# Kernel optimization log

Hardware: AMD Instinct MI355X
Metric: run time of the kernel (lower is better)

The kernel has to match this reference:

```python
import jax, jax.numpy as jnp
import numpy as np

EPS = 1e-5

def _ln(v, g, b):
    m = v.mean(-1, keepdims=True)
    var = ((v - m) ** 2).mean(-1, keepdims=True)
    return (v - m) * jax.lax.rsqrt(var + EPS) * g + b

def _causal_dwconv(x, w, b):
    # x: [B,S,C], w: [C,K] depthwise kernel, b: [C]; causal (left) padding
    K = w.shape[1]
    xt = x.transpose(0, 2, 1)  # [B,C,S]
    out = jax.lax.conv_general_dilated(xt, w[:, None, :], (1,), [(K - 1, 0)],
                                       dimension_numbers=('NCH', 'OIH', 'NCH'),
                                       feature_group_count=w.shape[0])
    return out.transpose(0, 2, 1) + b

def _ssm_scan(dt, Bm, Cm, x, A):
    # dt,x: [B,S,Di]; Bm,Cm: [B,S,N]; A: [Di,N] -> y: [B,S,Di]
    def step(h, inp):
        dt_t, B_t, C_t, x_t = inp
        dA = jnp.exp(dt_t[..., None] * A)                      # [B,Di,N]
        h = dA * h + dt_t[..., None] * B_t[:, None, :] * x_t[..., None]
        return h, jnp.einsum('bdn,bn->bd', h, C_t)
    h0 = jnp.zeros((dt.shape[0], A.shape[0], A.shape[1]), dt.dtype)
    xs = (dt.swapaxes(0, 1), Bm.swapaxes(0, 1), Cm.swapaxes(0, 1), x.swapaxes(0, 1))
    _, ys = jax.lax.scan(step, h0, xs)
    return ys.swapaxes(0, 1)

def _mamba_block(u, g, b, iW, cW, cB, xW, dW, dB, Al, Dpar, oW):
    # MambaBlock: LN -> Mamba -> residual
    Di, N = Al.shape
    R = dW.shape[1]
    xn = _ln(u, g, b)
    xz = xn @ iW.T                                  # [B,S,2*Di]
    xc, z = xz[..., :Di], xz[..., Di:]
    xc = jax.nn.silu(_causal_dwconv(xc, cW, cB))
    dbl = xc @ xW.T                                 # [B,S,R+2N]
    dt = jax.nn.softplus(dbl[..., :R] @ dW.T + dB)
    Bm, Cm = dbl[..., R:R + N], dbl[..., R + N:]
    A = -jnp.exp(Al)
    y = _ssm_scan(dt, Bm, Cm, xc, A) + xc * Dpar
    y = y * jax.nn.silu(z)
    return u + y @ oW.T

def _encoder(x, ln_g, ln_b, inW, convW, convB, xprojW, dtW, dtB, A_log, Dp, outW,
             ipW, ipB, opW, opB, fln_g, fln_b):
    L = ln_g.shape[0]
    h = x
    for i in range(L):
        xp = h @ ipW[i].T + ipB[i]
        Dh = xp.shape[-1] // 2
        yf = _mamba_block(xp[..., :Dh], ln_g[i, 0], ln_b[i, 0], inW[i, 0], convW[i, 0],
                          convB[i, 0], xprojW[i, 0], dtW[i, 0], dtB[i, 0], A_log[i, 0],
                          Dp[i, 0], outW[i, 0])
        xb_rev = jnp.flip(xp[..., Dh:], axis=1)
        yb = jnp.flip(_mamba_block(xb_rev, ln_g[i, 1], ln_b[i, 1], inW[i, 1], convW[i, 1],
                                   convB[i, 1], xprojW[i, 1], dtW[i, 1], dtB[i, 1],
                                   A_log[i, 1], Dp[i, 1], outW[i, 1]), axis=1)
        h = jnp.concatenate([yf, yb], axis=-1) @ opW[i].T + opB[i]
        # dropout is identity in eval mode
    return _ln(h, fln_g, fln_b)

def setup_inputs() -> dict:
    key = jax.random.key(0)
    L, B, S, D = 2, 2, 1024, 512
    Dh, Di, N, K, R = 256, 512, 16, 4, 16
    ks = jax.random.split(key, 9)
    s = 0.02
    x = jax.random.normal(ks[0], (B, S, D), jnp.float32)
    inW = jax.random.normal(ks[1], (L, 2, 2 * Di, Dh)) * s
    convW = jax.random.normal(ks[2], (L, 2, Di, K)) * 0.2
    xprojW = jax.random.normal(ks[3], (L, 2, R + 2 * N, Di)) * s
    dtW = jax.random.normal(ks[4], (L, 2, Di, R)) * (R ** -0.5)
    u = jax.random.uniform(ks[5], (L, 2, Di))
    dt = jnp.exp(u * (np.log(0.1) - np.log(0.001)) + np.log(0.001))
    dtB = dt + jnp.log(-jnp.expm1(-dt))          # inverse softplus init
    A_log = jnp.log(jnp.broadcast_to(jnp.arange(1, N + 1, dtype=jnp.float32), (L, 2, Di, N)))
    outW = jax.random.normal(ks[6], (L, 2, Dh, Di)) * s
    ipW = jax.random.normal(ks[7], (L, D, D)) * s
    opW = jax.random.normal(ks[8], (L, D, D)) * s
    return dict(x=x, ln_g=jnp.ones((L, 2, Dh)), ln_b=jnp.zeros((L, 2, Dh)), inW=inW,
                convW=convW, convB=jnp.zeros((L, 2, Di)), xprojW=xprojW, dtW=dtW, dtB=dtB,
                A_log=A_log, Dp=jnp.ones((L, 2, Di)), outW=outW, ipW=ipW,
                ipB=jnp.zeros((L, D)), opW=opW, opB=jnp.zeros((L, D)),
                fln_g=jnp.ones((D,)), fln_b=jnp.zeros((D,)))

def reference(x, ln_g, ln_b, inW, convW, convB, xprojW, dtW, dtB, A_log, Dp, outW,
              ipW, ipB, opW, opB, fln_g, fln_b):
    return _encoder(x, ln_g, ln_b, inW, convW, convB, xprojW, dtW, dtB, A_log, Dp, outW,
                    ipW, ipB, opW, opB, fln_g, fln_b)
```

## Files before the change

kernel.cpp:

```cpp
#include <hip/hip_runtime.h>
#include <hip/hip_bf16.h>
#include <math.h>

typedef __hip_bfloat16 bf16;
typedef __attribute__((ext_vector_type(8))) short s8v;
typedef __attribute__((ext_vector_type(4))) float f4v;

#define B_ 2
#define S_ 1024
#define D_ 512
#define DH_ 256
#define DI_ 512
#define N_ 16
#define M_ 2048
#define M2_ 4096
#define T_ 16
#define CN_ 64
#define NCP_ 640

#define IPW_N (2*512*512)
#define INW_N (4*1024*256)
#define OUTW_N (4*256*512)
#define OPW_N (2*512*512)
#define PREP_R0 ((IPW_N+INW_N+OUTW_N+OPW_N)/4)
#define PREP_R1 (4*NCP_*512)
#define PREP_R2 ((M_*D_)/4)

__device__ __forceinline__ float softplus_fast(float v) {
  return (v > 15.f) ? v : __logf(1.f + __expf(v));
}

__global__ __launch_bounds__(256) void k_prep_all(
    const float* __restrict__ ipW, const float* __restrict__ inW,
    const float* __restrict__ outW, const float* __restrict__ opW,
    const float* __restrict__ dtW, const float* __restrict__ xprojW,
    const float* __restrict__ x,
    bf16* __restrict__ ipWb, bf16* __restrict__ inWb,
    bf16* __restrict__ outWb, bf16* __restrict__ opWb,
    bf16* __restrict__ Wcomb, bf16* __restrict__ xb) {
  int i = blockIdx.x * 256 + threadIdx.x;
  if (i < PREP_R0) {
    int e = i * 4;
    const float* s; bf16* dst; int off;
    if (e < IPW_N)                       { s = ipW;  dst = ipWb;  off = e; }
    else if (e < IPW_N + INW_N)          { s = inW;  dst = inWb;  off = e - IPW_N; }
    else if (e < IPW_N + INW_N + OUTW_N) { s = outW; dst = outWb; off = e - IPW_N - INW_N; }
    else                                 { s = opW;  dst = opWb;  off = e - IPW_N - INW_N - OUTW_N; }
    float4 v = *(const float4*)&s[off];
    dst[off + 0] = __float2bfloat16(v.x);
    dst[off + 1] = __float2bfloat16(v.y);
    dst[off + 2] = __float2bfloat16(v.z);
    dst[off + 3] = __float2bfloat16(v.w);
  } else if (i < PREP_R0 + PREP_R1) {
    int idx = i - PREP_R0;
    int k = idx & 511;
    int row = (idx >> 9) % NCP_;
    int wi = idx / (NCP_ * 512);
    float v = 0.f;
    if (row < 512) {
      const float* dw = dtW + (size_t)wi * 512 * 16 + row * 16;
      const float* xw = xprojW + (size_t)wi * 48 * 512;
#pragma unroll
      for (int r = 0; r < 16; r++) v += dw[r] * xw[r * 512 + k];
    } else if (row < 544) {
      v = xprojW[(size_t)wi * 48 * 512 + (16 + row - 512) * 512 + k];
    }
    Wcomb[idx] = __float2bfloat16(v);
  } else if (i < PREP_R0 + PREP_R1 + PREP_R2) {
    int e = (i - PREP_R0 - PREP_R1) * 4;
    float4 v = *(const float4*)&x[e];
    xb[e + 0] = __float2bfloat16(v.x);
    xb[e + 1] = __float2bfloat16(v.y);
    xb[e + 2] = __float2bfloat16(v.z);
    xb[e + 3] = __float2bfloat16(v.w);
  }
}

__global__ __launch_bounds__(256) void k_mgX(
    const bf16* __restrict__ A, const bf16* __restrict__ W, long Wstr,
    const float* __restrict__ bias, int bstr,
    float* __restrict__ C, bf16* __restrict__ Cb, int ldc, int K, int ep) {
  __shared__ short As[64][40];
  __shared__ short Ws[128][40];
  const int bm = blockIdx.y * 64, bn = blockIdx.x * 128;
  const int seg = bm >> 11;
  const bf16* Wp = W + (size_t)seg * Wstr;
  const float* bp = bias ? bias + (size_t)seg * bstr : nullptr;
  const int tid = threadIdx.x;
  const int wave = tid >> 6, lane = tid & 63;
  const int q = lane >> 4, l15 = lane & 15;
  const int wc = wave * 32;
  const int arow = tid >> 2, acol = (tid & 3) * 8;
  const int wrow = tid >> 1, wcol = (tid & 1) * 16;

  f4v acc[4][2];
#pragma unroll
  for (int s = 0; s < 4; s++)
#pragma unroll
    for (int j = 0; j < 2; j++) acc[s][j] = (f4v){0.f, 0.f, 0.f, 0.f};

  for (int k0 = 0; k0 < K; k0 += 32) {
    *(uint4*)&As[arow][acol] = *(const uint4*)&A[(size_t)(bm + arow) * K + k0 + acol];
    const bf16* wsrc = &Wp[(size_t)(bn + wrow) * K + k0 + wcol];
    *(uint4*)&Ws[wrow][wcol] = *(const uint4*)wsrc;
    *(uint4*)&Ws[wrow][wcol + 8] = *(const uint4*)(wsrc + 8);
    __syncthreads();
    s8v af[4], bf[2];
#pragma unroll
    for (int s = 0; s < 4; s++) af[s] = *(const s8v*)&As[s * 16 + l15][q * 8];
#pragma unroll
    for (int j = 0; j < 2; j++) bf[j] = *(const s8v*)&Ws[wc + j * 16 + l15][q * 8];
#pragma unroll
    for (int s = 0; s < 4; s++)
#pragma unroll
      for (int j = 0; j < 2; j++)
        acc[s][j] = __builtin_amdgcn_mfma_f32_16x16x32_bf16(af[s], bf[j], acc[s][j], 0, 0, 0);
    __syncthreads();
  }
#pragma unroll
  for (int j = 0; j < 2; j++) {
    int col = bn + wc + j * 16 + l15;
#pragma unroll
    for (int s = 0; s < 4; s++) {
      int row0 = bm + s * 16 + q * 4;
#pragma unroll
      for (int r = 0; r < 4; r++) {
        float v = acc[s][j][r];
        if (ep == 1) {
          Cb[(size_t)(row0 + r) * ldc + col] = __float2bfloat16(v);
        } else {
          if (col < 512) v = softplus_fast(v + bp[col]);
          C[(size_t)(row0 + r) * ldc + col] = v;
        }
      }
    }
  }
}

__global__ __launch_bounds__(256) void k_mgemm(
    const bf16* __restrict__ A, const float* __restrict__ Af,
    const bf16* __restrict__ W, long Wstr,
    const float* __restrict__ bias, int bstr,
    const float* res,
    float* C, bf16* Cb, int ldc, int K, int ep) {
  __shared__ short As[64][40];
  __shared__ short Ws[64][40];
  const int bm = blockIdx.y * 64, bn = blockIdx.x * 64;
  const int seg = bm >> 11;
  const bf16* Wp = W + (size_t)seg * Wstr;
  const float* bp = bias ? bias + (size_t)seg * bstr : nullptr;
  const int tid = threadIdx.x;
  const int wave = tid >> 6, lane = tid & 63;
  const int q = lane >> 4, l15 = lane & 15;
  const int trow = tid >> 2, tcol = (tid & 3) * 8;

  f4v acc[4];
#pragma unroll
  for (int s = 0; s < 4; s++) acc[s] = (f4v){0.f, 0.f, 0.f, 0.f};

  for (int k0 = 0; k0 < K; k0 += 32) {
    if (ep == 4) {
      int ck = k0 + tcol;
      const float* src = (ck < 256)
          ? Af + (size_t)(bm + trow) * 256 + ck
          : Af + (size_t)M_ * 256 + (size_t)((bm + trow) ^ 1023) * 256 + (ck - 256);
      float4 f0 = *(const float4*)src;
      float4 f1 = *(const float4*)(src + 4);
      float fv[8] = {f0.x, f0.y, f0.z, f0.w, f1.x, f1.y, f1.z, f1.w};
      short tmp[8];
#pragma unroll
      for (int i = 0; i < 8; i++) {
        bf16 b = __float2bfloat16(fv[i]);
        tmp[i] = *(short*)&b;
      }
      *(uint4*)&As[trow][tcol] = *(uint4*)tmp;
    } else {
      *(uint4*)&As[trow][tcol] = *(const uint4*)&A[(size_t)(bm + trow) * K + k0 + tcol];
    }
    *(uint4*)&Ws[trow][tcol] = *(const uint4*)&Wp[(size_t)(bn + trow) * K + k0 + tcol];
    __syncthreads();
    s8v bfrag = *(const s8v*)&Ws[wave * 16 + l15][q * 8];
#pragma unroll
    for (int s = 0; s < 4; s++) {
      s8v afrag = *(const s8v*)&As[s * 16 + l15][q * 8];
      acc[s] = __builtin_amdgcn_mfma_f32_16x16x32_bf16(afrag, bfrag, acc[s], 0, 0, 0);
    }
    __syncthreads();
  }
  const int col = bn + wave * 16 + l15;
#pragma unroll
  for (int s = 0; s < 4; s++) {
#pragma unroll
    for (int r = 0; r < 4; r++) {
      int row = bm + s * 16 + q * 4 + r;
      float v = acc[s][r];
      if (ep == 0) {
        if (bp) v += bp[col];
        if (res) v += res[(size_t)row * ldc + col];
        C[(size_t)row * ldc + col] = v;
      } else if (ep == 3) {
        v += bp[col];
        if (col < 256)
          C[(size_t)row * 256 + col] = v;
        else
          C[(size_t)M_ * 256 + (size_t)(row ^ 1023) * 256 + (col - 256)] = v;
      } else {
        v += bp[col];
        C[(size_t)row * 512 + col] = v;
        Cb[(size_t)row * 512 + col] = __float2bfloat16(v);
      }
    }
  }
}

__global__ __launch_bounds__(256) void k_ln(const float* __restrict__ X,
                                            const float* __restrict__ g,
                                            const float* __restrict__ bta,
                                            int gstr, void* __restrict__ Y,
                                            int C, int out_bf16) {
  const int row = blockIdx.x;
  const int sel = (row >= M_) ? gstr : 0;
  const float* xr = X + (size_t)row * C;
  const int tid = threadIdx.x;
  const int per = C >> 8;
  float vals[2];
  float sum = 0.f, sumsq = 0.f;
  for (int i = 0; i < per; i++) {
    float v = xr[tid + i * 256];
    vals[i] = v;
    sum += v;
    sumsq += v * v;
  }
#pragma unroll
  for (int off = 1; off < 64; off <<= 1) {
    sum += __shfl_xor(sum, off, 64);
    sumsq += __shfl_xor(sumsq, off, 64);
  }
  __shared__ float s1[4], s2[4];
  int wid = tid >> 6, lane = tid & 63;
  if (lane == 0) { s1[wid] = sum; s2[wid] = sumsq; }
  __syncthreads();
  if (tid == 0) {
    float a = 0.f, c2 = 0.f;
    for (int w = 0; w < 4; w++) { a += s1[w]; c2 += s2[w]; }
    s1[0] = a; s2[0] = c2;
  }
  __syncthreads();
  float mean = s1[0] / (float)C;
  float var = s2[0] / (float)C - mean * mean;
  float rstd = rsqrtf(var + 1e-5f);
  for (int i = 0; i < per; i++) {
    int c = tid + i * 256;
    float y = (vals[i] - mean) * rstd * g[sel + c] + bta[sel + c];
    if (out_bf16)
      ((bf16*)Y)[(size_t)row * C + c] = __float2bfloat16(y);
    else
      ((float*)Y)[(size_t)row * C + c] = y;
  }
}

__global__ __launch_bounds__(256) void k_conv(const bf16* __restrict__ xz,
                                              const float* __restrict__ convW,
                                              const float* __restrict__ convB,
                                              bf16* __restrict__ outb) {
  int idx = blockIdx.x * 256 + threadIdx.x;
  if (idx >= M2_ * DI_) return;
  int d = idx & (DI_ - 1);
  int row = idx >> 9;
  int seg = row >> 11;
  int t = row & (S_ - 1);
  const float* w = convW + seg * DI_ * 4;
  float acc = convB[seg * DI_ + d];
#pragma unroll
  for (int k = 0; k < 4; k++) {
    int dt_ = k - 3;
    if (t + dt_ >= 0)
      acc += w[d * 4 + k] * __bfloat162float(xz[(size_t)(row + dt_) * 1024 + d]);
  }
  float s = acc / (1.f + __expf(-acc));
  outb[idx] = __float2bfloat16(s);
}

__global__ __launch_bounds__(256) void k_scanA(
    const float* __restrict__ dtbc,
    const bf16* __restrict__ xcb,
    const float* __restrict__ A_log,
    float* __restrict__ P,
    float* __restrict__ hend) {
  const int blk = blockIdx.x;
  const int half = blk & 1;
  const int c = (blk >> 1) & (CN_ - 1);
  const int s = blk >> 7;
  const int dir = s >> 1;
  const int d = half * 256 + threadIdx.x;
  const int r0 = s * S_ + c * T_;
  __shared__ float Bs[T_][16];
  for (int i = threadIdx.x; i < T_ * 16; i += 256) {
    int t = i >> 4, n = i & 15;
    Bs[t][n] = dtbc[(size_t)(r0 + t) * NCP_ + 512 + n];
  }
  float Av[16];
#pragma unroll
  for (int n = 0; n < 16; n++) Av[n] = -__expf(A_log[dir * DI_ * 16 + d * 16 + n]);
  float dtv[T_], xv[T_];
#pragma unroll
  for (int t = 0; t < T_; t++) {
    size_t row = (size_t)(r0 + t);
    dtv[t] = dtbc[row * NCP_ + d];
    xv[t]  = __bfloat162float(xcb[row * 512 + d]);
  }
  __syncthreads();
  float h[16], Pr[16];
#pragma unroll
  for (int n = 0; n < 16; n++) { h[n] = 0.f; Pr[n] = 1.f; }
#pragma unroll
  for (int t = 0; t < T_; t++) {
    float dtx = dtv[t] * xv[t];
#pragma unroll
    for (int n = 0; n < 16; n++) {
      float a = __expf(dtv[t] * Av[n]);
      h[n] = a * h[n] + dtx * Bs[t][n];
      Pr[n] *= a;
    }
  }
  size_t base = (((size_t)s * CN_ + c) * 16) * 512 + d;
#pragma unroll
  for (int n = 0; n < 16; n++) {
    P[base + (size_t)n * 512] = Pr[n];
    hend[base + (size_t)n * 512] = h[n];
  }
}

__global__ __launch_bounds__(256) void k_scanB(
    const float* __restrict__ P,
    const float* __restrict__ hend,
    float* __restrict__ Hinit) {
  int idx = blockIdx.x * 256 + threadIdx.x;
  if (idx >= 4 * 16 * 512) return;
  int d = idx & 511;
  int n = (idx >> 9) & 15;
  int s = idx >> 13;
  float H = 0.f;
  for (int c = 0; c < CN_; c++) {
    size_t o = (((size_t)s * CN_ + c) * 16 + n) * 512 + d;
    float p = P[o];
    float he = hend[o];
    Hinit[o] = H;
    H = p * H + he;
  }
}

__global__ __launch_bounds__(256) void k_scanC(
    const float* __restrict__ dtbc,
    const bf16* __restrict__ xz,
    const bf16* __restrict__ xcb,
    const float* __restrict__ A_log,
    const float* __restrict__ Dp,
    const float* __restrict__ Hinit,
    bf16* __restrict__ ybf) {
  const int blk = blockIdx.x;
  const int half = blk & 1;
  const int c = (blk >> 1) & (CN_ - 1);
  const int s = blk >> 7;
  const int dir = s >> 1;
  const int d = half * 256 + threadIdx.x;
  const int r0 = s * S_ + c * T_;
  __shared__ float Bs[T_][16], Cs[T_][16];
  for (int i = threadIdx.x; i < T_ * 16; i += 256) {
    int t = i >> 4, n = i & 15;
    size_t ro = (size_t)(r0 + t) * NCP_;
    Bs[t][n] = dtbc[ro + 512 + n];
    Cs[t][n] = dtbc[ro + 528 + n];
  }
  float Av[16];
#pragma unroll
  for (int n = 0; n < 16; n++) Av[n] = -__expf(A_log[dir * DI_ * 16 + d * 16 + n]);
  float Dd = Dp[dir * DI_ + d];
  float dtv[T_], xv[T_], zv[T_];
#pragma unroll
  for (int t = 0; t < T_; t++) {
    size_t row = (size_t)(r0 + t);
    dtv[t] = dtbc[row * NCP_ + d];
    xv[t]  = __bfloat162float(xcb[row * 512 + d]);
    zv[t]  = __bfloat162float(xz[row * 1024 + 512 + d]);
  }
  float h[16];
  size_t hbase = (((size_t)s * CN_ + c) * 16) * 512 + d;
#pragma unroll
  for (int n = 0; n < 16; n++) h[n] = Hinit[hbase + (size_t)n * 512];
  __syncthreads();
#pragma unroll
  for (int t = 0; t < T_; t++) {
    float dtx = dtv[t] * xv[t];
    float acc = 0.f;
#pragma unroll
    for (int n = 0; n < 16; n++) {
      float a = __expf(dtv[t] * Av[n]);
      h[n] = a * h[n] + dtx * Bs[t][n];
      acc += h[n] * Cs[t][n];
    }
    float sil = zv[t] / (1.f + __expf(-zv[t]));
    ybf[(size_t)(r0 + t) * 512 + d] = __float2bfloat16((acc + xv[t] * Dd) * sil);
  }
}

extern "C" void kernel_launch(void* const* d_in, const int* in_sizes, int n_in,
                              void* d_out, int out_size, void* d_ws, size_t ws_size,
                              hipStream_t stream) {
  const float* x     = (const float*)d_in[0];
  const float* ln_g  = (const float*)d_in[1];
  const float* ln_b  = (const float*)d_in[2];
  const float* inW   = (const float*)d_in[3];
  const float* convW = (const float*)d_in[4];
  const float* convB = (const float*)d_in[5];
  const float* xprojW= (const float*)d_in[6];
  const float* dtW   = (const float*)d_in[7];
  const float* dtB   = (const float*)d_in[8];
  const float* A_log = (const float*)d_in[9];
  const float* Dp    = (const float*)d_in[10];
  const float* outW  = (const float*)d_in[11];
  const float* ipW   = (const float*)d_in[12];
  const float* ipB   = (const float*)d_in[13];
  const float* opW   = (const float*)d_in[14];
  const float* opB   = (const float*)d_in[15];
  const float* fln_g = (const float*)d_in[16];
  const float* fln_b = (const float*)d_in[17];
  float* out = (float*)d_out;

  float* w = (float*)d_ws;
  float* h_cur = w;  w += (size_t)M_ * D_;
  float* u_f   = w;  w += (size_t)M2_ * DH_;
  float* dtbc2 = w;  w += (size_t)M2_ * NCP_;
  float* Pbuf  = w;  w += (size_t)4 * CN_ * 16 * 512;
  float* hend  = w;  w += (size_t)4 * CN_ * 16 * 512;
  float* Hinit = Pbuf;
  bf16* bw = (bf16*)w;
  bf16* xz2b  = bw;  bw += (size_t)M2_ * 1024;
  bf16* xb    = bw;  bw += (size_t)M_ * D_;
  bf16* xnb2  = bw;  bw += (size_t)M2_ * DH_;
  bf16* xcvb2 = bw;  bw += (size_t)M2_ * DI_;
  bf16* ybf2  = bw;  bw += (size_t)M2_ * DI_;
  bf16* ipWb  = bw;  bw += (size_t)IPW_N;
  bf16* inWb  = bw;  bw += (size_t)INW_N;
  bf16* outWb = bw;  bw += (size_t)OUTW_N;
  bf16* opWb  = bw;  bw += (size_t)OPW_N;
  bf16* Wcomb = bw;  bw += (size_t)4 * NCP_ * 512;

  int prep_threads = PREP_R0 + PREP_R1 + PREP_R2;
  k_prep_all<<<(prep_threads + 255) / 256, 256, 0, stream>>>(
      ipW, inW, outW, opW, dtW, xprojW, x,
      ipWb, inWb, outWb, opWb, Wcomb, xb);

  for (int li = 0; li < 2; li++) {
    k_mgemm<<<dim3(8, 32), 256, 0, stream>>>(
        xb, nullptr, ipWb + (size_t)li * D_ * D_, 0,
        ipB + (size_t)li * D_, 0, nullptr, u_f, nullptr, 256, D_, 3);
    k_ln<<<M2_, 256, 0, stream>>>(u_f, ln_g + li * 2 * DH_, ln_b + li * 2 * DH_,
                                  DH_, (void*)xnb2, DH_, 1);
    k_mgX<<<dim3(8, 64), 256, 0, stream>>>(
        xnb2, inWb + (size_t)li * 2 * 1024 * DH_, (long)1024 * DH_,
        nullptr, 0, nullptr, xz2b, 1024, DH_, 1);
    k_conv<<<(M2_ * DI_ + 255) / 256, 256, 0, stream>>>(
        xz2b, convW + li * 2 * DI_ * 4, convB + li * 2 * DI_, xcvb2);
    k_mgX<<<dim3(NCP_ / 128, 64), 256, 0, stream>>>(
        xcvb2, Wcomb + (size_t)li * 2 * NCP_ * 512, (long)NCP_ * 512,
        dtB + li * 2 * DI_, DI_, dtbc2, nullptr, NCP_, 512, 2);
    k_scanA<<<4 * CN_ * 2, 256, 0, stream>>>(
        dtbc2, xcvb2, A_log + (size_t)li * 2 * DI_ * N_, Pbuf, hend);
    k_scanB<<<(4 * 16 * 512 + 255) / 256, 256, 0, stream>>>(Pbuf, hend, Hinit);
    k_scanC<<<4 * CN_ * 2, 256, 0, stream>>>(
        dtbc2, xz2b, xcvb2, A_log + (size_t)li * 2 * DI_ * N_,
        Dp + (size_t)li * 2 * DI_, Hinit, ybf2);
    k_mgemm<<<dim3(4, 64), 256, 0, stream>>>(
        ybf2, nullptr, outWb + (size_t)li * 2 * DH_ * DI_, (long)DH_ * DI_,
        nullptr, 0, u_f, u_f, nullptr, 256, DI_, 0);
    k_mgemm<<<dim3(8, 32), 256, 0, stream>>>(
        nullptr, u_f, opWb + (size_t)li * D_ * D_, 0,
        opB + (size_t)li * D_, 0, nullptr, h_cur, xb, 512, D_, 4);
  }
  k_ln<<<M_, 256, 0, stream>>>(h_cur, fln_g, fln_b, 0, (void*)out, D_, 0);
}
```

Measured before the change: 363.5 us.

## Register-prefetch next K tile in GEMMs and halve N tile for more blocks

```diff
diff --git a/kernel.cpp b/kernel.cpp
--- a/kernel.cpp
+++ b/kernel.cpp
@@ -99,12 +99,22 @@
 #pragma unroll
     for (int j = 0; j < 2; j++) acc[s][j] = (f4v){0.f, 0.f, 0.f, 0.f};
 
+  uint4 a_reg = *(const uint4*)&A[(size_t)(bm + arow) * K + acol];
+  const bf16* wsrc0 = &Wp[(size_t)(bn + wrow) * K + wcol];
+  uint4 w_reg0 = *(const uint4*)wsrc0;
+  uint4 w_reg1 = *(const uint4*)(wsrc0 + 8);
+
   for (int k0 = 0; k0 < K; k0 += 32) {
-    *(uint4*)&As[arow][acol] = *(const uint4*)&A[(size_t)(bm + arow) * K + k0 + acol];
-    const bf16* wsrc = &Wp[(size_t)(bn + wrow) * K + k0 + wcol];
-    *(uint4*)&Ws[wrow][wcol] = *(const uint4*)wsrc;
-    *(uint4*)&Ws[wrow][wcol + 8] = *(const uint4*)(wsrc + 8);
+    *(uint4*)&As[arow][acol] = a_reg;
+    *(uint4*)&Ws[wrow][wcol] = w_reg0;
+    *(uint4*)&Ws[wrow][wcol + 8] = w_reg1;
     __syncthreads();
+    if (k0 + 32 < K) {
+      a_reg = *(const uint4*)&A[(size_t)(bm + arow) * K + k0 + 32 + acol];
+      const bf16* wsrc = &Wp[(size_t)(bn + wrow) * K + k0 + 32 + wcol];
+      w_reg0 = *(const uint4*)wsrc;
+      w_reg1 = *(const uint4*)(wsrc + 8);
+    }
     s8v af[4], bf[2];
 #pragma unroll
     for (int s = 0; s < 4; s++) af[s] = *(const s8v*)&As[s * 16 + l15][q * 8];
@@ -137,15 +147,15 @@
   }
 }
 
-__global__ __launch_bounds__(256) void k_mgemm(
+__global__ __launch_bounds__(256) void k_mg32(
     const bf16* __restrict__ A, const float* __restrict__ Af,
     const bf16* __restrict__ W, long Wstr,
     const float* __restrict__ bias, int bstr,
     const float* res,
     float* C, bf16* Cb, int ldc, int K, int ep) {
   __shared__ short As[64][40];
-  __shared__ short Ws[64][40];
-  const int bm = blockIdx.y * 64, bn = blockIdx.x * 64;
+  __shared__ short Ws[32][40];
+  const int bm = blockIdx.y * 64, bn = blockIdx.x * 32;
   const int seg = bm >> 11;
   const bf16* Wp = W + (size_t)seg * Wstr;
   const float* bp = bias ? bias + (size_t)seg * bstr : nullptr;
@@ -153,14 +163,16 @@
   const int wave = tid >> 6, lane = tid & 63;
   const int q = lane >> 4, l15 = lane & 15;
   const int trow = tid >> 2, tcol = (tid & 3) * 8;
-
-  f4v acc[4];
-#pragma unroll
-  for (int s = 0; s < 4; s++) acc[s] = (f4v){0.f, 0.f, 0.f, 0.f};
-
-  for (int k0 = 0; k0 < K; k0 += 32) {
+  const bool wact = tid < 128;
+
+  f4v acc[2];
+  acc[0] = (f4v){0.f, 0.f, 0.f, 0.f};
+  acc[1] = (f4v){0.f, 0.f, 0.f, 0.f};
+
+  uint4 a_reg, w_reg;
+  {
     if (ep == 4) {
-      int ck = k0 + tcol;
+      int ck = tcol;
       const float* src = (ck < 256)
           ? Af + (size_t)(bm + trow) * 256 + ck
           : Af + (size_t)M_ * 256 + (size_t)((bm + trow) ^ 1023) * 256 + (ck - 256);
@@ -169,31 +181,51 @@
       float fv[8] = {f0.x, f0.y, f0.z, f0.w, f1.x, f1.y, f1.z, f1.w};
       short tmp[8];
 #pragma unroll
-      for (int i = 0; i < 8; i++) {
-        bf16 b = __float2bfloat16(fv[i]);
-        tmp[i] = *(short*)&b;
+      for (int i = 0; i < 8; i++) { bf16 b = __float2bfloat16(fv[i]); tmp[i] = *(short*)&b; }
+      a_reg = *(uint4*)tmp;
+    } else {
+      a_reg = *(const uint4*)&A[(size_t)(bm + trow) * K + tcol];
+    }
+    if (wact) w_reg = *(const uint4*)&Wp[(size_t)(bn + trow) * K + tcol];
+  }
+
+  for (int k0 = 0; k0 < K; k0 += 32) {
+    *(uint4*)&As[trow][tcol] = a_reg;
+    if (wact) *(uint4*)&Ws[trow][tcol] = w_reg;
+    __syncthreads();
+    if (k0 + 32 < K) {
+      int kn = k0 + 32;
+      if (ep == 4) {
+        int ck = kn + tcol;
+        const float* src = (ck < 256)
+            ? Af + (size_t)(bm + trow) * 256 + ck
+            : Af + (size_t)M_ * 256 + (size_t)((bm + trow) ^ 1023) * 256 + (ck - 256);
+        float4 f0 = *(const float4*)src;
+        float4 f1 = *(const float4*)(src + 4);
+        float fv[8] = {f0.x, f0.y, f0.z, f0.w, f1.x, f1.y, f1.z, f1.w};
+        short tmp[8];
+#pragma unroll
+        for (int i = 0; i < 8; i++) { bf16 b = __float2bfloat16(fv[i]); tmp[i] = *(short*)&b; }
+        a_reg = *(uint4*)tmp;
+      } else {
+        a_reg = *(const uint4*)&A[(size_t)(bm + trow) * K + kn + tcol];
       }
-      *(uint4*)&As[trow][tcol] = *(uint4*)tmp;
-    } else {
-      *(uint4*)&As[trow][tcol] = *(const uint4*)&A[(size_t)(bm + trow) * K + k0 + tcol];
-    }
-    *(uint4*)&Ws[trow][tcol] = *(const uint4*)&Wp[(size_t)(bn + trow) * K + k0 + tcol];
+      if (wact) w_reg = *(const uint4*)&Wp[(size_t)(bn + trow) * K + kn + tcol];
+    }
+    s8v afrag = *(const s8v*)&As[wave * 16 + l15][q * 8];
+    s8v bf0 = *(const s8v*)&Ws[l15][q * 8];
+    s8v bf1 = *(const s8v*)&Ws[16 + l15][q * 8];
+    acc[0] = __builtin_amdgcn_mfma_f32_16x16x32_bf16(afrag, bf0, acc[0], 0, 0, 0);
+    acc[1] = __builtin_amdgcn_mfma_f32_16x16x32_bf16(afrag, bf1, acc[1], 0, 0, 0);
     __syncthreads();
-    s8v bfrag = *(const s8v*)&Ws[wave * 16 + l15][q * 8];
-#pragma unroll
-    for (int s = 0; s < 4; s++) {
-      s8v afrag = *(const s8v*)&As[s * 16 + l15][q * 8];
-      acc[s] = __builtin_amdgcn_mfma_f32_16x16x32_bf16(afrag, bfrag, acc[s], 0, 0, 0);
-    }
-    __syncthreads();
-  }
-  const int col = bn + wave * 16 + l15;
-#pragma unroll
-  for (int s = 0; s < 4; s++) {
+  }
+#pragma unroll
+  for (int j = 0; j < 2; j++) {
+    int col = bn + j * 16 + l15;
 #pragma unroll
     for (int r = 0; r < 4; r++) {
-      int row = bm + s * 16 + q * 4 + r;
-      float v = acc[s][r];
+      int row = bm + wave * 16 + q * 4 + r;
+      float v = acc[j][r];
       if (ep == 0) {
         if (bp) v += bp[col];
         if (res) v += res[(size_t)row * ldc + col];
@@ -452,7 +484,7 @@
       ipWb, inWb, outWb, opWb, Wcomb, xb);
 
   for (int li = 0; li < 2; li++) {
-    k_mgemm<<<dim3(8, 32), 256, 0, stream>>>(
+    k_mg32<<<dim3(16, 32), 256, 0, stream>>>(
         xb, nullptr, ipWb + (size_t)li * D_ * D_, 0,
         ipB + (size_t)li * D_, 0, nullptr, u_f, nullptr, 256, D_, 3);
     k_ln<<<M2_, 256, 0, stream>>>(u_f, ln_g + li * 2 * DH_, ln_b + li * 2 * DH_,
@@ -471,10 +503,10 @@
     k_scanC<<<4 * CN_ * 2, 256, 0, stream>>>(
         dtbc2, xz2b, xcvb2, A_log + (size_t)li * 2 * DI_ * N_,
         Dp + (size_t)li * 2 * DI_, Hinit, ybf2);
-    k_mgemm<<<dim3(4, 64), 256, 0, stream>>>(
+    k_mg32<<<dim3(8, 64), 256, 0, stream>>>(
         ybf2, nullptr, outWb + (size_t)li * 2 * DH_ * DI_, (long)DH_ * DI_,
         nullptr, 0, u_f, u_f, nullptr, 256, DI_, 0);
-    k_mgemm<<<dim3(8, 32), 256, 0, stream>>>(
+    k_mg32<<<dim3(16, 32), 256, 0, stream>>>(
         nullptr, u_f, opWb + (size_t)li * D_ * D_, 0,
         opB + (size_t)li * D_, 0, nullptr, h_cur, xb, 512, D_, 4);
   }
```

New measurement: 330.9 us. 1.1x faster.
